# Optimization experiments

Hardware: AMD Instinct MI355X
Metric: run time of the kernel (lower is better)

Reference implementation:

```python
import jax, jax.numpy as jnp
import numpy as np

B, IN, H = 1024, 2048, 2048
W_BIT = A_BIT = I_BIT = R_BIT = 8


def fake_quant(x, bits):
    # brevitas CommonQuant: signed, narrow-range, const scale 1.0 ->
    # int scale s = 1/(2^(b-1)-1); q = clip(round(x/s), -n, n); dq = q*s.
    n = 2.0 ** (bits - 1) - 1.0
    q = jnp.clip(x * n, -n, n)
    q = q + jax.lax.stop_gradient(jnp.round(q) - q)  # STE round
    return q / n


def setup_inputs() -> dict:
    key = jax.random.key(0)
    ks = jax.random.split(key, 7)
    std = 1.0 / np.sqrt(H)  # reset_parameters: uniform(-std, std)
    return {
        "x": jax.random.normal(ks[0], (B, IN), jnp.float32),
        "hx": jax.random.normal(ks[1], (B, H), jnp.float32),
        "cx": jax.random.normal(ks[2], (B, H), jnp.float32),
        "w_x2h": jax.random.uniform(ks[3], (4 * H, IN), jnp.float32, -std, std),
        "b_x2h": jax.random.uniform(ks[4], (4 * H,), jnp.float32, -std, std),
        "w_h2h": jax.random.uniform(ks[5], (4 * H, H), jnp.float32, -std, std),
        "b_h2h": jax.random.uniform(ks[6], (4 * H,), jnp.float32, -std, std),
    }


def reference(x, hx, cx, w_x2h, b_x2h, w_h2h, b_h2h):
    x_q = fake_quant(x, I_BIT)                      # input_quant
    wx_q = fake_quant(w_x2h, W_BIT)                 # CommonWeightQuant
    wh_q = fake_quant(w_h2h, W_BIT)
    gates = (jnp.einsum('bi,gi->bg', x_q, wx_q) + b_x2h
             + jnp.einsum('bh,gh->bg', hx, wh_q) + b_h2h)  # [B, 4H]
    f, i, g, o = jnp.split(gates, 4, axis=1)        # forget, input, cell, out
    f = fake_quant(jax.nn.sigmoid(f), A_BIT)
    i = fake_quant(jax.nn.sigmoid(i), A_BIT)
    g = fake_quant(jnp.tanh(g), A_BIT)
    o = fake_quant(jax.nn.sigmoid(o), A_BIT)
    c_new = f * cx + i * g
    h_new = o * fake_quant(jnp.tanh(c_new), A_BIT)
    c_out = fake_quant(c_new, R_BIT)                # recurrent_quant
    return (h_new, c_out)
```

## Files before the change

kernel.cpp:

```cpp
#include <hip/hip_runtime.h>
#include <stdint.h>
#include <math.h>

typedef __attribute__((ext_vector_type(4))) int i32x4;
typedef __attribute__((ext_vector_type(4))) float f32x4;

#define GLD16(gp, lp)                                                     \
  __builtin_amdgcn_global_load_lds(                                       \
      (__attribute__((address_space(1))) void*)(gp),                      \
      (__attribute__((address_space(3))) void*)(lp), 16, 0, 0)

__global__ void __launch_bounds__(256) k_prep_w(const float* __restrict__ wx,
                                                const float* __restrict__ wh,
                                                signed char* __restrict__ Wq) {
  int i = blockIdx.x * 256 + threadIdx.x;
  int e = i << 2;
  int g = e >> 12;
  int c = e & 4095;
  const float* src = (c < 2048) ? (wx + g * 2048 + c) : (wh + g * 2048 + (c - 2048));
  float4 v = *(const float4*)src;
  char4 o;
  o.x = (signed char)(int)rint(fmin(fmax((double)v.x * 127.0, -127.0), 127.0));
  o.y = (signed char)(int)rint(fmin(fmax((double)v.y * 127.0, -127.0), 127.0));
  o.z = (signed char)(int)rint(fmin(fmax((double)v.z * 127.0, -127.0), 127.0));
  o.w = (signed char)(int)rint(fmin(fmax((double)v.w * 127.0, -127.0), 127.0));
  *(char4*)(Wq + e) = o;
}

__global__ void __launch_bounds__(256) k_prep_a(const float* __restrict__ x,
                                                const float* __restrict__ hx,
                                                signed char* __restrict__ Aq) {
  int i = blockIdx.x * 256 + threadIdx.x;
  int e = i << 2;
  int b = e >> 11;
  int c = e & 2047;
  float4 xv = *(const float4*)(x + b * 2048 + c);
  float4 hv = *(const float4*)(hx + b * 2048 + c);
  float xa[4] = {xv.x, xv.y, xv.z, xv.w};
  float ha[4] = {hv.x, hv.y, hv.z, hv.w};
  char4 q4, s1, s2, s3, s4, s5;
  signed char* qp = (signed char*)&q4;
  signed char* p1 = (signed char*)&s1;
  signed char* p2 = (signed char*)&s2;
  signed char* p3 = (signed char*)&s3;
  signed char* p4 = (signed char*)&s4;
  signed char* p5 = (signed char*)&s5;
  #pragma unroll
  for (int j = 0; j < 4; ++j) {
    qp[j] = (signed char)(int)rint(fmin(fmax((double)xa[j] * 127.0, -127.0), 127.0));
    double r = (double)ha[j];
    double d1 = rint(r * 16.0);     r -= d1 * 0x1p-4;
    double d2 = rint(r * 0x1p11);   r -= d2 * 0x1p-11;
    double d3 = rint(r * 0x1p18);   r -= d3 * 0x1p-18;
    double d4 = rint(r * 0x1p25);   r -= d4 * 0x1p-25;
    double d5 = rint(r * 0x1p32);
    p1[j] = (signed char)(int)d1;
    p2[j] = (signed char)(int)d2;
    p3[j] = (signed char)(int)d3;
    p4[j] = (signed char)(int)d4;
    p5[j] = (signed char)(int)d5;
  }
  size_t base = (size_t)b * 12288;
  *(char4*)(Aq + base + 0 * 2048 + c) = s5;
  *(char4*)(Aq + base + 1 * 2048 + c) = s4;
  *(char4*)(Aq + base + 2 * 2048 + c) = s3;
  *(char4*)(Aq + base + 3 * 2048 + c) = s2;
  *(char4*)(Aq + base + 4 * 2048 + c) = s1;
  *(char4*)(Aq + base + 5 * 2048 + c) = q4;
}

__global__ void __launch_bounds__(256, 3) k_gemm_lstm(
    const signed char* __restrict__ Aq, const signed char* __restrict__ Wq,
    const float* __restrict__ bx, const float* __restrict__ bh,
    const float* __restrict__ cx, float* __restrict__ out) {
  __shared__ __align__(16) signed char smem[49152];

  const int t  = threadIdx.x;
  const int wv = t >> 6;
  const int ln = t & 63;
  const int wm = wv & 1;
  const int wn = wv >> 1;
  const int lr = ln & 15;
  const int q  = ln >> 4;

  const int j0 = blockIdx.x * 16;
  const int m0 = blockIdx.y * 128;

  int sA[4];
  #pragma unroll
  for (int is = 0; is < 4; ++is) {
    int s = is * 256 + t;
    int r = s >> 3;
    int c = s & 7;
    int cp = c ^ (r & 7);
    sA[is] = (m0 + r) * 12288 + cp * 16;
  }
  int sB[2];
  #pragma unroll
  for (int is = 0; is < 2; ++is) {
    int s = is * 256 + t;
    int r = s >> 3;
    int c = s & 7;
    int cp = c ^ (r & 7);
    int wrow = (r >> 4) * 2048 + j0 + (r & 15);
    sB[is] = wrow * 4096 + cp * 16;
  }

  int aoff[4], boff[2];
  const int swz = lr & 7;
  #pragma unroll
  for (int mf = 0; mf < 4; ++mf)
    aoff[mf] = (wm * 64 + mf * 16 + lr) * 128 + ((q ^ swz) * 16);
  #pragma unroll
  for (int nf = 0; nf < 2; ++nf)
    boff[nf] = (wn * 32 + nf * 16 + lr) * 128 + ((q ^ swz) * 16);

  i32x4 acc[4][2];
  f32x4 Hh[4][2], Hl[4][2];
  #pragma unroll
  for (int mf = 0; mf < 4; ++mf)
    #pragma unroll
    for (int nf = 0; nf < 2; ++nf)
      acc[mf][nf] = (i32x4){0, 0, 0, 0};

  {
    #pragma unroll
    for (int is = 0; is < 4; ++is)
      GLD16(Aq + sA[is], smem + is * 4096 + wv * 1024);
    #pragma unroll
    for (int is = 0; is < 2; ++is)
      GLD16(Wq + sB[is] + 2048, smem + 16384 + is * 4096 + wv * 1024);
  }
  asm volatile("s_waitcnt vmcnt(0)" ::: "memory");
  __syncthreads();

  int lbase = 0;
  #pragma unroll 1
  for (int g = 0; g < 96; ++g) {
    if (g < 95) {
      const int gn  = g + 1;
      const int phn = gn >> 4;
      const int kkn = (gn & 15) << 7;
      const int kAn = phn * 2048 + kkn;
      const int kBn = ((phn < 5) ? 2048 : 0) + kkn;
      const int nb  = lbase ^ 24576;
      #pragma unroll
      for (int is = 0; is < 4; ++is)
        GLD16(Aq + sA[is] + kAn, smem + nb + is * 4096 + wv * 1024);
      #pragma unroll
      for (int is = 0; is < 2; ++is)
        GLD16(Wq + sB[is] + kBn, smem + nb + 16384 + is * 4096 + wv * 1024);
    }

    const signed char* As = smem + lbase;
    const signed char* Bs = smem + lbase + 16384;
    #pragma unroll
    for (int s = 0; s < 2; ++s) {
      const int sx = s << 6;
      i32x4 af[4], bf[2];
      #pragma unroll
      for (int mf = 0; mf < 4; ++mf) af[mf] = *(const i32x4*)&As[aoff[mf] ^ sx];
      #pragma unroll
      for (int nf = 0; nf < 2; ++nf) bf[nf] = *(const i32x4*)&Bs[boff[nf] ^ sx];
      #pragma unroll
      for (int mf = 0; mf < 4; ++mf)
        #pragma unroll
        for (int nf = 0; nf < 2; ++nf)
          acc[mf][nf] = __builtin_amdgcn_mfma_i32_16x16x64_i8(
              af[mf], bf[nf], acc[mf][nf], 0, 0, 0);
    }

    if ((g & 15) == 15) {
      const int ph = g >> 4;
      if (ph == 0) {
        #pragma unroll
        for (int mf = 0; mf < 4; ++mf)
          #pragma unroll
          for (int nf = 0; nf < 2; ++nf) {
            #pragma unroll
            for (int r = 0; r < 4; ++r) {
              Hh[mf][nf][r] = (float)acc[mf][nf][r];
              Hl[mf][nf][r] = 0.f;
            }
            acc[mf][nf] = (i32x4){0, 0, 0, 0};
          }
      } else if (ph < 5) {
        #pragma unroll
        for (int mf = 0; mf < 4; ++mf)
          #pragma unroll
          for (int nf = 0; nf < 2; ++nf) {
            #pragma unroll
            for (int r = 0; r < 4; ++r) {
              float tv = Hh[mf][nf][r] * 0x1p-7f;
              float S  = (float)acc[mf][nf][r];
              float sm = tv + S;
              float z  = sm - tv;
              float e  = (tv - (sm - z)) + (S - z);
              Hl[mf][nf][r] = Hl[mf][nf][r] * 0x1p-7f + e;
              Hh[mf][nf][r] = sm;
            }
            acc[mf][nf] = (i32x4){0, 0, 0, 0};
          }
      }
    }

    asm volatile("s_waitcnt vmcnt(0)" ::: "memory");
    __syncthreads();
    lbase ^= 24576;
  }

  const double invsq = 1.0 / 16129.0;
  const double hsc   = 0x1p-4 / 127.0;

  float (*Lgo)[128][17] = (float(*)[128][17])smem;

  if (wn == 1) {
    #pragma unroll
    for (int mf = 0; mf < 4; ++mf) {
      #pragma unroll
      for (int nf = 0; nf < 2; ++nf) {
        int gate = 2 + nf;
        int gcol = gate * 2048 + j0 + lr;
        double bsum = (double)bx[gcol] + (double)bh[gcol];
        #pragma unroll
        for (int r = 0; r < 4; ++r) {
          double Sx = (double)acc[mf][nf][r];
          double Hd = ((double)Hh[mf][nf][r] + (double)Hl[mf][nf][r]) * hsc;
          double pre = Sx * invsq + Hd + bsum;
          double av = (gate == 2) ? tanh(pre) : (1.0 / (1.0 + exp(-pre)));
          double qv = rint(fmin(fmax(av * 127.0, -127.0), 127.0));
          int m = wm * 64 + mf * 16 + q * 4 + r;
          Lgo[nf][m][lr] = (float)qv;
        }
      }
    }
  }
  __syncthreads();
  if (wn == 0) {
    #pragma unroll
    for (int mf = 0; mf < 4; ++mf) {
      int gcf = j0 + lr;
      int gci = 2048 + j0 + lr;
      double bf_ = (double)bx[gcf] + (double)bh[gcf];
      double bi_ = (double)bx[gci] + (double)bh[gci];
      #pragma unroll
      for (int r = 0; r < 4; ++r) {
        int m = wm * 64 + mf * 16 + q * 4 + r;
        double fpre = (double)acc[mf][0][r] * invsq +
                      ((double)Hh[mf][0][r] + (double)Hl[mf][0][r]) * hsc + bf_;
        double ipre = (double)acc[mf][1][r] * invsq +
                      ((double)Hh[mf][1][r] + (double)Hl[mf][1][r]) * hsc + bi_;
        double fs = 1.0 / (1.0 + exp(-fpre));
        double is = 1.0 / (1.0 + exp(-ipre));
        double fv = rint(fmin(fmax(fs * 127.0, -127.0), 127.0)) / 127.0;
        double iv = rint(fmin(fmax(is * 127.0, -127.0), 127.0)) / 127.0;
        double gv = (double)Lgo[0][m][lr] / 127.0;
        double ov = (double)Lgo[1][m][lr] / 127.0;
        int row = m0 + m;
        int col = j0 + lr;
        double cn = fv * (double)cx[row * 2048 + col] + iv * gv;
        double tq = rint(fmin(fmax(tanh(cn) * 127.0, -127.0), 127.0)) / 127.0;
        double hv = ov * tq;
        double cq = rint(fmin(fmax(cn * 127.0, -127.0), 127.0)) / 127.0;
        out[row * 2048 + col] = (float)hv;
        out[2097152 + row * 2048 + col] = (float)cq;
      }
    }
  }
}

extern "C" void kernel_launch(void* const* d_in, const int* in_sizes, int n_in,
                              void* d_out, int out_size, void* d_ws, size_t ws_size,
                              hipStream_t stream) {
  const float* x  = (const float*)d_in[0];
  const float* hx = (const float*)d_in[1];
  const float* cx = (const float*)d_in[2];
  const float* wx = (const float*)d_in[3];
  const float* bx = (const float*)d_in[4];
  const float* wh = (const float*)d_in[5];
  const float* bh = (const float*)d_in[6];
  float* out = (float*)d_out;

  signed char* Wq = (signed char*)d_ws;
  signed char* Aq = (signed char*)d_ws + 33554432;

  k_prep_w<<<dim3(32768), dim3(256), 0, stream>>>(wx, wh, Wq);
  k_prep_a<<<dim3(2048), dim3(256), 0, stream>>>(x, hx, Aq);
  k_gemm_lstm<<<dim3(128, 8), dim3(256), 0, stream>>>(Aq, Wq, bx, bh, cx, out);
}
```

Baseline: 360.8 us.

## Deepen GEMM K-loop to three-stage LDS pipeline with partial vmcnt waits

Moves the int8 MFMA GEMM main loop from double buffering to a three-stage ring of LDS buffers. Loads are issued two iterations ahead, and each iteration waits only for the older batch (vmcnt(6)) instead of draining all outstanding loads. The aim is to hide global-to-LDS latency better. In exchange, shared memory grows to 72KB and the occupancy hint drops from 3 to 2 blocks per CU. A sync is added before the epilogue reuses the shared memory.

```diff
diff --git a/kernel.cpp b/kernel.cpp
--- a/kernel.cpp
+++ b/kernel.cpp
@@ -69,11 +69,11 @@
   *(char4*)(Aq + base + 5 * 2048 + c) = q4;
 }
 
-__global__ void __launch_bounds__(256, 3) k_gemm_lstm(
+__global__ void __launch_bounds__(256, 2) k_gemm_lstm(
     const signed char* __restrict__ Aq, const signed char* __restrict__ Wq,
     const float* __restrict__ bx, const float* __restrict__ bh,
     const float* __restrict__ cx, float* __restrict__ out) {
-  __shared__ __align__(16) signed char smem[49152];
+  __shared__ __align__(16) signed char smem[73728];
 
   const int t  = threadIdx.x;
   const int wv = t >> 6;
@@ -130,30 +130,37 @@
     #pragma unroll
     for (int is = 0; is < 2; ++is)
       GLD16(Wq + sB[is] + 2048, smem + 16384 + is * 4096 + wv * 1024);
-  }
-  asm volatile("s_waitcnt vmcnt(0)" ::: "memory");
-  __syncthreads();
-
-  int lbase = 0;
+    #pragma unroll
+    for (int is = 0; is < 4; ++is)
+      GLD16(Aq + sA[is] + 128, smem + 24576 + is * 4096 + wv * 1024);
+    #pragma unroll
+    for (int is = 0; is < 2; ++is)
+      GLD16(Wq + sB[is] + 2048 + 128, smem + 24576 + 16384 + is * 4096 + wv * 1024);
+  }
+  asm volatile("s_waitcnt vmcnt(6)" ::: "memory");
+  __builtin_amdgcn_s_barrier();
+  __builtin_amdgcn_sched_barrier(0);
+
+  int cur = 0;
+  int stg = 49152;
   #pragma unroll 1
   for (int g = 0; g < 96; ++g) {
-    if (g < 95) {
-      const int gn  = g + 1;
+    if (g < 94) {
+      const int gn  = g + 2;
       const int phn = gn >> 4;
       const int kkn = (gn & 15) << 7;
       const int kAn = phn * 2048 + kkn;
       const int kBn = ((phn < 5) ? 2048 : 0) + kkn;
-      const int nb  = lbase ^ 24576;
       #pragma unroll
       for (int is = 0; is < 4; ++is)
-        GLD16(Aq + sA[is] + kAn, smem + nb + is * 4096 + wv * 1024);
+        GLD16(Aq + sA[is] + kAn, smem + stg + is * 4096 + wv * 1024);
       #pragma unroll
       for (int is = 0; is < 2; ++is)
-        GLD16(Wq + sB[is] + kBn, smem + nb + 16384 + is * 4096 + wv * 1024);
-    }
-
-    const signed char* As = smem + lbase;
-    const signed char* Bs = smem + lbase + 16384;
+        GLD16(Wq + sB[is] + kBn, smem + stg + 16384 + is * 4096 + wv * 1024);
+    }
+
+    const signed char* As = smem + cur;
+    const signed char* Bs = smem + cur + 16384;
     #pragma unroll
     for (int s = 0; s < 2; ++s) {
       const int sx = s << 6;
@@ -204,9 +211,16 @@
       }
     }
 
-    asm volatile("s_waitcnt vmcnt(0)" ::: "memory");
-    __syncthreads();
-    lbase ^= 24576;
+    if (g < 94) {
+      asm volatile("s_waitcnt vmcnt(6)" ::: "memory");
+    } else {
+      asm volatile("s_waitcnt vmcnt(0)" ::: "memory");
+    }
+    __builtin_amdgcn_sched_barrier(0);
+    __builtin_amdgcn_s_barrier();
+    __builtin_amdgcn_sched_barrier(0);
+    cur += 24576; if (cur == 73728) cur = 0;
+    stg += 24576; if (stg == 73728) stg = 0;
   }
 
   const double invsq = 1.0 / 16129.0;
@@ -214,6 +228,7 @@
 
   float (*Lgo)[128][17] = (float(*)[128][17])smem;
 
+  __syncthreads();
   if (wn == 1) {
     #pragma unroll
     for (int mf = 0; mf < 4; ++mf) {
```

Measured after the change: 351.2 us. 1.03x faster.
